# Kernel tuning notes

Hardware: AMD Instinct MI355X
Metric: run time of the kernel (lower is better)

## Reference

```python
import jax, jax.numpy as jnp
import numpy as np

EPS = 1e-3  # matches eps=0.001 in __init__


def p2o(psf, H, W):
    """PSF -> OTF: zero-pad to (H,W), roll so kernel center is at origin, FFT2."""
    B, C, kh, kw = psf.shape
    otf = jnp.zeros((B, C, H, W), psf.dtype).at[:, :, :kh, :kw].set(psf)
    otf = jnp.roll(otf, (-(kh // 2), -(kw // 2)), axis=(-2, -1))
    return jnp.fft.fft2(otf)


def splits_mean(a, sf):
    """Mean over the sf*sf distinct blocks of splits(): contiguous-chunk split
    via view(sf, H/sf, sf, W/sf); mean over the two sf axes equals mean over
    the scale^2 trailing dim of the original splits output."""
    B, C, H, W = a.shape
    return a.reshape(B, C, sf, H // sf, sf, W // sf).mean(axis=(2, 4))


def setup_inputs() -> dict:
    key = jax.random.key(0)
    kx, kk = jax.random.split(key)
    x = jax.random.normal(kx, (4, 64, 128, 128), dtype=jnp.float32)
    k = jax.random.uniform(kk, (4, 64, 25, 25), dtype=jnp.float32)
    alpha = jnp.zeros((1, 64, 1, 1), dtype=jnp.float32)  # learned parameter
    return {"x": x, "k": k, "alpha": alpha, "sf": 2}


def reference(x, k, alpha, sf):
    biaseps = jax.nn.sigmoid(alpha - 9.0) + EPS          # (1,C,1,1)
    B, C, h, w = x.shape
    H, W = h * sf, w * sf
    # s-fold zero-fill upsample (STy)
    STy = jnp.zeros((B, C, H, W), x.dtype).at[:, :, ::sf, ::sf].set(x)
    # nearest-neighbor interpolate by sf
    xu = jnp.repeat(jnp.repeat(x, sf, axis=-2), sf, axis=-1) if sf != 1 else x
    FB = p2o(k, H, W)                                    # complex (B,C,H,W)
    FBC = jnp.conj(FB)
    F2B = jnp.abs(FB) ** 2
    FBFy = FBC * jnp.fft.fft2(STy)
    FR = FBFy + jnp.fft.fft2(biaseps * xu)
    FBR = splits_mean(FB * FR, sf)                       # (B,C,H/sf,W/sf)
    invW = splits_mean(F2B, sf)
    invWBR = FBR / (invW + biaseps)
    FCBinvWBR = FBC * jnp.tile(invWBR, (1, 1, sf, sf))   # repeat(1,1,sf,sf)
    FX = (FR - FCBinvWBR) / biaseps
    return jnp.real(jnp.fft.ifft2(FX))
```

## Files before the change

kernel.cpp:

```cpp
#include <hip/hip_runtime.h>
#include <math.h>


static __device__ __forceinline__ float2 cmul(float2 a, float2 b) {
    return make_float2(a.x * b.x - a.y * b.y, a.x * b.y + a.y * b.x);
}
static __device__ __forceinline__ float2 cadd(float2 a, float2 b) {
    return make_float2(a.x + b.x, a.y + b.y);
}
static __device__ __forceinline__ float2 csub(float2 a, float2 b) {
    return make_float2(a.x - b.x, a.y - b.y);
}
static __device__ __forceinline__ float2 conjf2(float2 a) {
    return make_float2(a.x, -a.y);
}
static __device__ __forceinline__ int PHI(int i) { return i + (i >> 3); }

template <int HB, int SIGN, int THREADS>
static __device__ __forceinline__ void fill_tw(float2* tw) {
    for (int i = threadIdx.x; i < HB; i += THREADS) {
        float s, c;
        __sincosf((float)SIGN * (float)M_PI * (float)i / (float)HB, &s, &c);
        tw[i] = make_float2(c, s);
    }
}

template <int N, int R, int SIGN>
static __device__ __forceinline__ int fft_lds_rows(float2 (&buf)[2][R][N],
                                                   const float2* __restrict__ tw) {
    constexpr int HB = N / 2;
    const int tid = threadIdx.x;
    const int row = tid / HB;
    const int bt = tid % HB;
    int cur = 0, m = 1;
    for (int l = HB; l >= 1; l >>= 1) {
        __syncthreads();
        const int k = bt & (m - 1);
        const float2 w = tw[bt - k];
        float2 a = buf[cur][row][bt];
        float2 b = buf[cur][row][bt + HB];
        float2 d = make_float2(a.x - b.x, a.y - b.y);
        float2 wd = make_float2(w.x * d.x - w.y * d.y, w.x * d.y + w.y * d.x);
        const int o = 2 * bt - k;
        buf[cur ^ 1][row][o] = make_float2(a.x + b.x, a.y + b.y);
        buf[cur ^ 1][row][o + m] = wd;
        cur ^= 1;
        m <<= 1;
    }
    __syncthreads();
    return cur;
}

template <int SIGN, int NCOL>
static __device__ __forceinline__ int fft4_cols_wavelocal(float2 (&buf)[2][NCOL][130],
                                                          const float2* __restrict__ tw) {
    const int lane = threadIdx.x & 63;
    const int wv = threadIdx.x >> 6;
    const int col = wv * 4 + (lane >> 4);
    const int r = lane & 15;
    int cur = 0, m = 1;
#pragma unroll
    for (int st = 0; st < 3; ++st) {
#pragma unroll
        for (int b = 0; b < 2; ++b) {
            const int bq = r + 16 * b;
            const int k = bq & (m - 1);
            const int jm = bq - k;
            const float2 w1 = tw[jm];
            const float2 w2 = tw[2 * jm];
            const float2 w3 = tw[3 * jm];
            float2 a0 = buf[cur][col][bq];
            float2 a1 = buf[cur][col][bq + 32];
            float2 a2 = buf[cur][col][bq + 64];
            float2 a3 = buf[cur][col][bq + 96];
            float2 s02 = cadd(a0, a2), d02 = csub(a0, a2);
            float2 s13 = cadd(a1, a3), d13 = csub(a1, a3);
            float2 b0 = cadd(s02, s13), b2 = csub(s02, s13);
            float2 b1 = make_float2(d02.x - (float)SIGN * d13.y,
                                    d02.y + (float)SIGN * d13.x);
            float2 b3 = make_float2(d02.x + (float)SIGN * d13.y,
                                    d02.y - (float)SIGN * d13.x);
            const int o = 4 * jm + k;
            buf[cur ^ 1][col][o] = b0;
            buf[cur ^ 1][col][o + m] = cmul(w1, b1);
            buf[cur ^ 1][col][o + 2 * m] = cmul(w2, b2);
            buf[cur ^ 1][col][o + 3 * m] = cmul(w3, b3);
        }
        cur ^= 1;
        m <<= 2;
    }
#pragma unroll
    for (int b = 0; b < 4; ++b) {
        const int bt = r + 16 * b;
        float2 a = buf[cur][col][bt];
        float2 bb = buf[cur][col][bt + 64];
        buf[cur ^ 1][col][bt] = cadd(a, bb);
        buf[cur ^ 1][col][bt + 64] = csub(a, bb);
    }
    return cur ^ 1;
}

__global__ __launch_bounds__(256) void k1_fft_rows_x(const float* __restrict__ x,
                                                     float2* __restrict__ Fx) {
    __shared__ float2 buf[2][4][128];
    __shared__ float2 tw64m[64];
    const int tid = threadIdx.x;
    const int row = tid >> 6;
    const int t = tid & 63;
    fill_tw<64, -1, 256>(tw64m);
    const int gpair = blockIdx.x * 4 + row;
    const float* r0 = x + (size_t)gpair * 256;
    const float* r1 = r0 + 128;
    const float2 a0 = ((const float2*)r0)[t];
    const float2 a1 = ((const float2*)r1)[t];
    buf[0][row][2 * t].x = a0.x;
    buf[0][row][2 * t].y = a1.x;
    buf[0][row][2 * t + 1].x = a0.y;
    buf[0][row][2 * t + 1].y = a1.y;
    int cur = fft_lds_rows<128, 4, -1>(buf, tw64m);
    float2* d0 = Fx + (size_t)gpair * 256;
    float2* d1 = d0 + 128;
    for (int h = 0; h < 2; ++h) {
        int tt = t + h * 64;
        if (tt > 64) continue;
        float2 Zt = buf[cur][row][tt];
        float2 Zm = buf[cur][row][(128 - tt) & 127];
        d0[tt] = make_float2(0.5f * (Zt.x + Zm.x), 0.5f * (Zt.y - Zm.y));
        float ax = Zt.x - Zm.x, ay = Zt.y + Zm.y;
        d1[tt] = make_float2(0.5f * ay, -0.5f * ax);
    }
}

__global__ __launch_bounds__(256) void k2_fft_cols_x(float2* __restrict__ Fx) {
    __shared__ float2 buf[2][16][130];
    __shared__ float2 tw[96];
    const int tid = threadIdx.x;
    const int img = blockIdx.x / 5;
    const int c0 = (blockIdx.x % 5) * 16;
    for (int i = tid; i < 96; i += 256) {
        float s, c;
        __sincosf(-(float)M_PI * (float)i / 64.f, &s, &c);
        tw[i] = make_float2(c, s);
    }
    float2* base = Fx + (size_t)img * 16384 + c0;
    for (int it = 0; it < 8; ++it) {
        int idx = it * 256 + tid;
        int rr = idx >> 4, cc = idx & 15;
        buf[0][cc][rr] = base[rr * 128 + cc];
    }
    __syncthreads();
    int cur = fft4_cols_wavelocal<-1, 16>(buf, tw);
    __syncthreads();
    for (int it = 0; it < 8; ++it) {
        int idx = it * 256 + tid;
        int rr = idx >> 4, cc = idx & 15;
        base[rr * 128 + cc] = buf[cur][cc][rr];
    }
}

__global__ __launch_bounds__(128) void k3_fft_rows_k(const float* __restrict__ kin,
                                                     float2* __restrict__ FBtmp) {
    __shared__ float2 buf[2][1][256];
    __shared__ float2 tw128m[128];
    const int tid = threadIdx.x;
    const int img = blockIdx.x / 25;
    const int lr = blockIdx.x % 25;
    fill_tw<128, -1, 128>(tw128m);
    const float* krow = kin + img * 625 + lr * 25;
    for (int h = 0; h < 2; ++h) {
        int v = tid + h * 128;
        int pc = (v + 12) & 255;
        buf[0][0][v] = make_float2(pc < 25 ? krow[pc] : 0.f, 0.f);
    }
    int cur = fft_lds_rows<256, 1, -1>(buf, tw128m);
    float2* dst = FBtmp + (size_t)img * 6400 + lr * 256;
    dst[tid] = buf[cur][0][tid];
    dst[tid + 128] = buf[cur][0][tid + 128];
}

__global__ __launch_bounds__(256, 4) void k6_fused(const float2* __restrict__ FBtmp,
                                                   const float2* __restrict__ Fx,
                                                   const float* __restrict__ alpha,
                                                   float2* __restrict__ Zf) {
    __shared__ float2 sm_buf0[4 * 288];
    __shared__ float2 sm_buf1[4 * 288];
    __shared__ float2 tw[192];
    float2* Tt = sm_buf0;
    float2* stageF = sm_buf1;
    const int tid = threadIdx.x;
    const int rs = tid >> 6;
    const int q = tid & 63;
    const int img = blockIdx.x / 33;
    const int bq = blockIdx.x % 33;
    const int pa = 2 * bq;
    const int pb = (pa + 1 < 65) ? (pa + 1) : 64;

    const float2* src = FBtmp + (size_t)img * 6400 + tid;
    float2 S[25];
#pragma unroll
    for (int p = 0; p < 25; ++p) S[p] = src[p * 256];

    for (int i = tid; i < 192; i += 256) {
        float s, c;
        __sincosf((float)M_PI * (float)i / 128.f, &s, &c);
        tw[i] = make_float2(c, s);
    }
    {
        const float k2pi = -2.f * (float)M_PI / 256.f;
        for (int i = tid; i < 50; i += 256) {
            const int which = i / 25, p = i - which * 25;
            const int u = which ? pb : pa;
            float s, c;
            __sincosf(k2pi * (float)((u * (p + 244)) & 255), &s, &c);
            Tt[which * 25 + p] = make_float2(c, s);
        }
    }
    __syncthreads();

    {
        float2 aA = make_float2(0.f, 0.f), bA = make_float2(0.f, 0.f);
        float2 aB = make_float2(0.f, 0.f), bB = make_float2(0.f, 0.f);
#pragma unroll
        for (int p = 0; p < 25; ++p) {
            const float2 s = S[p];
            const float2 ta = Tt[p];
            const float axx = ta.x * s.x, ayy = ta.y * s.y;
            const float axy = ta.x * s.y, ayx = ta.y * s.x;
            aA.x += axx - ayy;
            aA.y += axy + ayx;
            if (p & 1) {
                bA.x -= axx + ayy;
                bA.y -= axy - ayx;
            } else {
                bA.x += axx + ayy;
                bA.y += axy - ayx;
            }
            const float2 tb = Tt[25 + p];
            const float bxx = tb.x * s.x, byy = tb.y * s.y;
            const float bxy = tb.x * s.y, byx = tb.y * s.x;
            aB.x += bxx - byy;
            aB.y += bxy + byx;
            if (p & 1) {
                bB.x -= bxx + byy;
                bB.y -= bxy - byx;
            } else {
                bB.x += bxx + byy;
                bB.y += bxy - byx;
            }
        }
        stageF[tid] = aA;
        stageF[256 + tid] = bA;
        stageF[512 + tid] = aB;
        stageF[768 + tid] = bB;
    }
    __syncthreads();

    const int p = (rs < 2) ? pa : pb;
    const int sb = rs & 2;
    const int u = ((rs & 1) == 0) ? p : (128 - p);
    const int um = u & 127;
    const int msel = (um == p) ? 0 : 1;
    const int mi = sb | msel;
    const int oi = sb | (1 - msel);

    const float ci = tw[um].x, si = -tw[um].y;
    const float b = 1.f / (1.f + __expf(9.f - alpha[img & 63])) + 1e-3f;
    const float scale = 1.f / 65536.f;
    const float2 Di0 = make_float2(1.f + ci, si);
    const float2 Di1 = make_float2(1.f - ci, -si);
    const float2 Du = (u < 128) ? Di0 : Di1;
#pragma unroll
    for (int h = 0; h < 2; ++h) {
        const int t = q + 64 * h;
        float2 f00 = stageF[mi * 256 + t];
        float2 f01 = stageF[mi * 256 + t + 128];
        float2 f10, f11;
        if (um == 0) {
            f10 = stageF[oi * 256 + t];
            f11 = stageF[oi * 256 + t + 128];
        } else {
            f10 = conjf2(stageF[oi * 256 + ((256 - t) & 255)]);
            f11 = conjf2(stageF[oi * 256 + 128 - t]);
        }
        const bool mir = (t > 64);
        const int rr = mir ? ((128 - um) & 127) : um;
        const int cc = mir ? (128 - t) : t;
        float2 fx = Fx[(size_t)img * 16384 + rr * 128 + cc];
        if (mir) fx.y = -fx.y;
        const float cj = tw[t].x, sj = -tw[t].y;
        float2 Dj0 = make_float2(1.f + cj, sj);
        float2 Dj1 = make_float2(1.f - cj, -sj);
        float2 A = cadd(cmul(f00, Dj0), cmul(f01, Dj1));
        float2 Bt = cadd(cmul(f10, Dj0), cmul(f11, Dj1));
        float2 S1 = cadd(cmul(A, Di0), cmul(Bt, Di1));
        S1.x *= 0.25f;
        S1.y *= 0.25f;
        float S2 = 0.25f * (f00.x * f00.x + f00.y * f00.y + f01.x * f01.x + f01.y * f01.y +
                            f10.x * f10.x + f10.y * f10.y + f11.x * f11.x + f11.y * f11.y);
        float inv = 1.f / (S2 + b);
        float2 mm = make_float2((1.f - S1.x) * inv, (-S1.y) * inv);
        float2 c0v = (u < 128) ? f00 : f10;
        float2 c1v = (u < 128) ? f01 : f11;
        float2 t0 = cadd(cmul(conjf2(c0v), mm), cmul(Du, Dj0));
        float2 t1 = cadd(cmul(conjf2(c1v), mm), cmul(Du, Dj1));
        float2 FX0 = cmul(fx, t0);
        float2 FX1 = cmul(fx, t1);
        sm_buf0[rs * 288 + PHI(t)] = make_float2(FX0.x * scale, FX0.y * scale);
        sm_buf0[rs * 288 + PHI(t + 128)] = make_float2(FX1.x * scale, FX1.y * scale);
    }
    __syncthreads();

    {
        float2* Bc = sm_buf0;
        float2* Bn = sm_buf1;
        int m = 1;
#pragma unroll
        for (int st = 0; st < 3; ++st) {
            const int k = q & (m - 1);
            const int jm = q - k;
            const float2 w1 = tw[jm];
            const float2 w2 = tw[2 * jm];
            const float2 w3 = tw[3 * jm];
            float2 a0 = Bc[rs * 288 + PHI(q)];
            float2 a1 = Bc[rs * 288 + PHI(q + 64)];
            float2 a2 = Bc[rs * 288 + PHI(q + 128)];
            float2 a3 = Bc[rs * 288 + PHI(q + 192)];
            float2 s02 = cadd(a0, a2), d02 = csub(a0, a2);
            float2 s13 = cadd(a1, a3), d13 = csub(a1, a3);
            float2 b0 = cadd(s02, s13), b2v = csub(s02, s13);
            float2 b1 = make_float2(d02.x - d13.y, d02.y + d13.x);
            float2 b3 = make_float2(d02.x + d13.y, d02.y - d13.x);
            const int o = 4 * jm + k;
            Bn[rs * 288 + PHI(o)] = b0;
            Bn[rs * 288 + PHI(o + m)] = cmul(w1, b1);
            Bn[rs * 288 + PHI(o + 2 * m)] = cmul(w2, b2v);
            Bn[rs * 288 + PHI(o + 3 * m)] = cmul(w3, b3);
            float2* tp = Bc; Bc = Bn; Bn = tp;
            m <<= 2;
        }
        {
            float2 a0 = Bc[rs * 288 + PHI(q)];
            float2 a1 = Bc[rs * 288 + PHI(q + 64)];
            float2 a2 = Bc[rs * 288 + PHI(q + 128)];
            float2 a3 = Bc[rs * 288 + PHI(q + 192)];
            float2 s02 = cadd(a0, a2), d02 = csub(a0, a2);
            float2 s13 = cadd(a1, a3), d13 = csub(a1, a3);
            Bc[rs * 288 + PHI(q)] = cadd(s02, s13);
            Bc[rs * 288 + PHI(q + 64)] = make_float2(d02.x - d13.y, d02.y + d13.x);
            Bc[rs * 288 + PHI(q + 128)] = csub(s02, s13);
            Bc[rs * 288 + PHI(q + 192)] = make_float2(d02.x + d13.y, d02.y - d13.x);
        }
    }
    __syncthreads();

    const int u0 = u;
    bool dowrite = ((rs & 1) == 0) ? true : (p > 0 && p < 64);
    if (pb == pa && rs >= 2) dowrite = false;
    if (dowrite) {
        const float2 w = tw[u0];
        float2* zb = Zf + (size_t)img * 32768 + (size_t)u0 * 256;
#pragma unroll
        for (int hh = 0; hh < 4; ++hh) {
            const int jj = q + 64 * hh;
            float2 su = sm_buf1[rs * 288 + PHI(jj)];
            float2 s2 = sm_buf1[(rs ^ 1) * 288 + PHI(jj)];
            float2 e = make_float2(su.x + s2.x, su.y - s2.y);
            float2 o_ = make_float2(su.x - s2.x, su.y + s2.y);
            float2 wo = cmul(w, o_);
            zb[jj] = make_float2(e.x - wo.y, e.y + wo.x);
        }
    }
}

__global__ __launch_bounds__(256) void k7_c2r(const float2* __restrict__ Zf,
                                              float* __restrict__ out) {
    __shared__ float2 buf[2][16][130];
    __shared__ float2 tw[96];
    const int tid = threadIdx.x;
    const int img = blockIdx.x >> 4;
    const int c0 = (blockIdx.x & 15) * 16;
    for (int i = tid; i < 96; i += 256) {
        float s, c;
        __sincosf((float)M_PI * (float)i / 64.f, &s, &c);
        tw[i] = make_float2(c, s);
    }
    const float2* zb = Zf + (size_t)img * 32768 + c0;
    for (int it = 0; it < 8; ++it) {
        int idx = it * 256 + tid;
        int rr = idx >> 4, cc = idx & 15;
        buf[0][cc][rr] = zb[rr * 256 + cc];
    }
    __syncthreads();
    int cur = fft4_cols_wavelocal<1, 16>(buf, tw);
    __syncthreads();
    float* ob = out + (size_t)img * 65536 + c0;
    for (int it = 0; it < 8; ++it) {
        int idx = it * 256 + tid;
        int n = idx >> 4, c = idx & 15;
        float2 y = buf[cur][c][n];
        ob[(2 * n) * 256 + c] = y.x;
        ob[(2 * n + 1) * 256 + c] = y.y;
    }
}

extern "C" void kernel_launch(void* const* d_in, const int* in_sizes, int n_in,
                              void* d_out, int out_size, void* d_ws, size_t ws_size,
                              hipStream_t stream) {
    const float* x = (const float*)d_in[0];
    const float* k = (const float*)d_in[1];
    const float* alpha = (const float*)d_in[2];
    float* out = (float*)d_out;

    float2* Fx = (float2*)d_ws;
    float2* Zf = Fx + 256 * 16384;
    float2* FBtmp = Zf + 256 * 32768;

    hipLaunchKernelGGL(k1_fft_rows_x, dim3(4096), dim3(256), 0, stream, x, Fx);
    hipLaunchKernelGGL(k2_fft_cols_x, dim3(256 * 5), dim3(256), 0, stream, Fx);
    hipLaunchKernelGGL(k3_fft_rows_k, dim3(6400), dim3(128), 0, stream, k, FBtmp);
    hipLaunchKernelGGL(k6_fused, dim3(256 * 33), dim3(256), 0, stream, FBtmp, Fx, alpha, Zf);
    hipLaunchKernelGGL(k7_c2r, dim3(4096), dim3(256), 0, stream, Zf, out);
}
```

Before: 181.3 us.

## Merge x-row and kernel-row FFT launches, register-fuse first FFT stage in k6

Fuses the row FFTs of x and of the PSF into one launch by splitting on block index, with two PSF rows per 256-thread block. This removes one kernel launch and the 128-thread small-block inefficiency. Inside k6_fused, the first radix-4 stage of the 256-point FFT now runs in registers straight from the computed spectrum values, with vectorised float4 LDS writes. It also drops the syncthreads between the later radix-4 stages, uses a new padding function, and reuses each thread's own results in registers during the final write. The wave-local stages without barriers rely on each row being handled by exactly one wavefront, and the k-path blocks do some dead work on padded rows.

```diff
diff --git a/kernel.cpp b/kernel.cpp
--- a/kernel.cpp
+++ b/kernel.cpp
@@ -14,7 +14,7 @@
 static __device__ __forceinline__ float2 conjf2(float2 a) {
     return make_float2(a.x, -a.y);
 }
-static __device__ __forceinline__ int PHI(int i) { return i + (i >> 3); }
+static __device__ __forceinline__ int PHI16(int i) { return i + ((i >> 4) << 1); }
 
 template <int HB, int SIGN, int THREADS>
 static __device__ __forceinline__ void fill_tw(float2* tw) {
@@ -100,34 +100,65 @@
     return cur ^ 1;
 }
 
-__global__ __launch_bounds__(256) void k1_fft_rows_x(const float* __restrict__ x,
-                                                     float2* __restrict__ Fx) {
-    __shared__ float2 buf[2][4][128];
-    __shared__ float2 tw64m[64];
+__global__ __launch_bounds__(256) void k13(const float* __restrict__ x,
+                                           const float* __restrict__ kin,
+                                           float2* __restrict__ Fx,
+                                           float2* __restrict__ FBtmp) {
+    __shared__ __align__(16) float2 pool[1152];
     const int tid = threadIdx.x;
-    const int row = tid >> 6;
-    const int t = tid & 63;
-    fill_tw<64, -1, 256>(tw64m);
-    const int gpair = blockIdx.x * 4 + row;
-    const float* r0 = x + (size_t)gpair * 256;
-    const float* r1 = r0 + 128;
-    const float2 a0 = ((const float2*)r0)[t];
-    const float2 a1 = ((const float2*)r1)[t];
-    buf[0][row][2 * t].x = a0.x;
-    buf[0][row][2 * t].y = a1.x;
-    buf[0][row][2 * t + 1].x = a0.y;
-    buf[0][row][2 * t + 1].y = a1.y;
-    int cur = fft_lds_rows<128, 4, -1>(buf, tw64m);
-    float2* d0 = Fx + (size_t)gpair * 256;
-    float2* d1 = d0 + 128;
-    for (int h = 0; h < 2; ++h) {
-        int tt = t + h * 64;
-        if (tt > 64) continue;
-        float2 Zt = buf[cur][row][tt];
-        float2 Zm = buf[cur][row][(128 - tt) & 127];
-        d0[tt] = make_float2(0.5f * (Zt.x + Zm.x), 0.5f * (Zt.y - Zm.y));
-        float ax = Zt.x - Zm.x, ay = Zt.y + Zm.y;
-        d1[tt] = make_float2(0.5f * ay, -0.5f * ax);
+    if (blockIdx.x < 4096) {
+        using Buf1 = float2[2][4][128];
+        Buf1& buf = *reinterpret_cast<Buf1*>(pool);
+        float2* tw64m = pool + 1024;
+        const int row = tid >> 6;
+        const int t = tid & 63;
+        fill_tw<64, -1, 256>(tw64m);
+        const int gpair = blockIdx.x * 4 + row;
+        const float* r0 = x + (size_t)gpair * 256;
+        const float* r1 = r0 + 128;
+        const float2 a0 = ((const float2*)r0)[t];
+        const float2 a1 = ((const float2*)r1)[t];
+        buf[0][row][2 * t].x = a0.x;
+        buf[0][row][2 * t].y = a1.x;
+        buf[0][row][2 * t + 1].x = a0.y;
+        buf[0][row][2 * t + 1].y = a1.y;
+        int cur = fft_lds_rows<128, 4, -1>(buf, tw64m);
+        float2* d0 = Fx + (size_t)gpair * 256;
+        float2* d1 = d0 + 128;
+        for (int h = 0; h < 2; ++h) {
+            int tt = t + h * 64;
+            if (tt > 64) continue;
+            float2 Zt = buf[cur][row][tt];
+            float2 Zm = buf[cur][row][(128 - tt) & 127];
+            d0[tt] = make_float2(0.5f * (Zt.x + Zm.x), 0.5f * (Zt.y - Zm.y));
+            float ax = Zt.x - Zm.x, ay = Zt.y + Zm.y;
+            d1[tt] = make_float2(0.5f * ay, -0.5f * ax);
+        }
+    } else {
+        using Buf3 = float2[2][2][256];
+        Buf3& buf = *reinterpret_cast<Buf3*>(pool);
+        float2* tw128m = pool + 1024;
+        const int b3 = blockIdx.x - 4096;
+        const int img = b3 / 13;
+        const int sub = b3 % 13;
+        const int row = tid >> 7;
+        const int t2 = tid & 127;
+        int lr = sub * 2 + row;
+        const bool live = (lr < 25);
+        if (!live) lr = 24;
+        fill_tw<128, -1, 256>(tw128m);
+        const float* krow = kin + img * 625 + lr * 25;
+        for (int h = 0; h < 2; ++h) {
+            int v = t2 + h * 128;
+            int pc = (v + 12) & 255;
+            buf[0][row][v] = make_float2(pc < 25 ? krow[pc] : 0.f, 0.f);
+        }
+        int cur = fft_lds_rows<256, 2, -1>(buf, tw128m);
+        if (live) {
+            float2* dst = FBtmp + (size_t)img * 6400 + lr * 256;
+            dst[t2] = buf[cur][row][t2];
+            dst[t2 + 128] = buf[cur][row][t2 + 128];
+        }
     }
 }
 
@@ -158,32 +189,12 @@
     }
 }
 
-__global__ __launch_bounds__(128) void k3_fft_rows_k(const float* __restrict__ kin,
-                                                     float2* __restrict__ FBtmp) {
-    __shared__ float2 buf[2][1][256];
-    __shared__ float2 tw128m[128];
-    const int tid = threadIdx.x;
-    const int img = blockIdx.x / 25;
-    const int lr = blockIdx.x % 25;
-    fill_tw<128, -1, 128>(tw128m);
-    const float* krow = kin + img * 625 + lr * 25;
-    for (int h = 0; h < 2; ++h) {
-        int v = tid + h * 128;
-        int pc = (v + 12) & 255;
-        buf[0][0][v] = make_float2(pc < 25 ? krow[pc] : 0.f, 0.f);
-    }
-    int cur = fft_lds_rows<256, 1, -1>(buf, tw128m);
-    float2* dst = FBtmp + (size_t)img * 6400 + lr * 256;
-    dst[tid] = buf[cur][0][tid];
-    dst[tid + 128] = buf[cur][0][tid + 128];
-}
-
 __global__ __launch_bounds__(256, 4) void k6_fused(const float2* __restrict__ FBtmp,
                                                    const float2* __restrict__ Fx,
                                                    const float* __restrict__ alpha,
                                                    float2* __restrict__ Zf) {
-    __shared__ float2 sm_buf0[4 * 288];
-    __shared__ float2 sm_buf1[4 * 288];
+    __shared__ __align__(16) float2 sm_buf0[4 * 288];
+    __shared__ __align__(16) float2 sm_buf1[4 * 288];
     __shared__ float2 tw[192];
     float2* Tt = sm_buf0;
     float2* stageF = sm_buf1;
@@ -269,6 +280,7 @@
     const float2 Di0 = make_float2(1.f + ci, si);
     const float2 Di1 = make_float2(1.f - ci, -si);
     const float2 Du = (u < 128) ? Di0 : Di1;
+    float2 X0, X1, X2, X3;
 #pragma unroll
     for (int h = 0; h < 2; ++h) {
         const int t = q + 64 * h;
@@ -305,52 +317,77 @@
         float2 t1 = cadd(cmul(conjf2(c1v), mm), cmul(Du, Dj1));
         float2 FX0 = cmul(fx, t0);
         float2 FX1 = cmul(fx, t1);
-        sm_buf0[rs * 288 + PHI(t)] = make_float2(FX0.x * scale, FX0.y * scale);
-        sm_buf0[rs * 288 + PHI(t + 128)] = make_float2(FX1.x * scale, FX1.y * scale);
-    }
-    __syncthreads();
-
-    {
-        float2* Bc = sm_buf0;
-        float2* Bn = sm_buf1;
-        int m = 1;
-#pragma unroll
-        for (int st = 0; st < 3; ++st) {
-            const int k = q & (m - 1);
-            const int jm = q - k;
-            const float2 w1 = tw[jm];
-            const float2 w2 = tw[2 * jm];
-            const float2 w3 = tw[3 * jm];
-            float2 a0 = Bc[rs * 288 + PHI(q)];
-            float2 a1 = Bc[rs * 288 + PHI(q + 64)];
-            float2 a2 = Bc[rs * 288 + PHI(q + 128)];
-            float2 a3 = Bc[rs * 288 + PHI(q + 192)];
-            float2 s02 = cadd(a0, a2), d02 = csub(a0, a2);
-            float2 s13 = cadd(a1, a3), d13 = csub(a1, a3);
-            float2 b0 = cadd(s02, s13), b2v = csub(s02, s13);
-            float2 b1 = make_float2(d02.x - d13.y, d02.y + d13.x);
-            float2 b3 = make_float2(d02.x + d13.y, d02.y - d13.x);
-            const int o = 4 * jm + k;
-            Bn[rs * 288 + PHI(o)] = b0;
-            Bn[rs * 288 + PHI(o + m)] = cmul(w1, b1);
-            Bn[rs * 288 + PHI(o + 2 * m)] = cmul(w2, b2v);
-            Bn[rs * 288 + PHI(o + 3 * m)] = cmul(w3, b3);
-            float2* tp = Bc; Bc = Bn; Bn = tp;
-            m <<= 2;
-        }
-        {
-            float2 a0 = Bc[rs * 288 + PHI(q)];
-            float2 a1 = Bc[rs * 288 + PHI(q + 64)];
-            float2 a2 = Bc[rs * 288 + PHI(q + 128)];
-            float2 a3 = Bc[rs * 288 + PHI(q + 192)];
-            float2 s02 = cadd(a0, a2), d02 = csub(a0, a2);
-            float2 s13 = cadd(a1, a3), d13 = csub(a1, a3);
-            Bc[rs * 288 + PHI(q)] = cadd(s02, s13);
-            Bc[rs * 288 + PHI(q + 64)] = make_float2(d02.x - d13.y, d02.y + d13.x);
-            Bc[rs * 288 + PHI(q + 128)] = csub(s02, s13);
-            Bc[rs * 288 + PHI(q + 192)] = make_float2(d02.x + d13.y, d02.y - d13.x);
-        }
-    }
+        FX0.x *= scale; FX0.y *= scale;
+        FX1.x *= scale; FX1.y *= scale;
+        if (h == 0) { X0 = FX0; X2 = FX1; } else { X1 = FX0; X3 = FX1; }
+    }
+
+    {
+        float2 s02 = cadd(X0, X2), d02 = csub(X0, X2);
+        float2 s13 = cadd(X1, X3), d13 = csub(X1, X3);
+        float2 b0 = cadd(s02, s13), b2v = csub(s02, s13);
+        float2 b1 = make_float2(d02.x - d13.y, d02.y + d13.x);
+        float2 b3 = make_float2(d02.x + d13.y, d02.y - d13.x);
+        float2 c1 = cmul(tw[q], b1);
+        float2 c2 = cmul(tw[2 * q], b2v);
+        float2 c3 = cmul(tw[3 * q], b3);
+        float4* dst4 = reinterpret_cast<float4*>(&sm_buf0[rs * 288 + PHI16(4 * q)]);
+        dst4[0] = make_float4(b0.x, b0.y, c1.x, c1.y);
+        dst4[1] = make_float4(c2.x, c2.y, c3.x, c3.y);
+    }
+    __syncthreads();
+
+    {
+        const int k4 = q & 3, jm = q - k4;
+        float2 a0 = sm_buf0[rs * 288 + PHI16(q)];
+        float2 a1 = sm_buf0[rs * 288 + PHI16(q + 64)];
+        float2 a2 = sm_buf0[rs * 288 + PHI16(q + 128)];
+        float2 a3 = sm_buf0[rs * 288 + PHI16(q + 192)];
+        float2 s02 = cadd(a0, a2), d02 = csub(a0, a2);
+        float2 s13 = cadd(a1, a3), d13 = csub(a1, a3);
+        float2 b0 = cadd(s02, s13), b2v = csub(s02, s13);
+        float2 b1 = make_float2(d02.x - d13.y, d02.y + d13.x);
+        float2 b3 = make_float2(d02.x + d13.y, d02.y - d13.x);
+        const int o = 4 * jm + k4;
+        sm_buf1[rs * 288 + PHI16(o)] = b0;
+        sm_buf1[rs * 288 + PHI16(o + 4)] = cmul(tw[jm], b1);
+        sm_buf1[rs * 288 + PHI16(o + 8)] = cmul(tw[2 * jm], b2v);
+        sm_buf1[rs * 288 + PHI16(o + 12)] = cmul(tw[3 * jm], b3);
+    }
+    {
+        const int k16 = q & 15, jm = q - k16;
+        float2 a0 = sm_buf1[rs * 288 + PHI16(q)];
+        float2 a1 = sm_buf1[rs * 288 + PHI16(q + 64)];
+        float2 a2 = sm_buf1[rs * 288 + PHI16(q + 128)];
+        float2 a3 = sm_buf1[rs * 288 + PHI16(q + 192)];
+        float2 s02 = cadd(a0, a2), d02 = csub(a0, a2);
+        float2 s13 = cadd(a1, a3), d13 = csub(a1, a3);
+        float2 b0 = cadd(s02, s13), b2v = csub(s02, s13);
+        float2 b1 = make_float2(d02.x - d13.y, d02.y + d13.x);
+        float2 b3 = make_float2(d02.x + d13.y, d02.y - d13.x);
+        const int o = 4 * jm + k16;
+        sm_buf0[rs * 288 + PHI16(o)] = b0;
+        sm_buf0[rs * 288 + PHI16(o + 16)] = cmul(tw[jm], b1);
+        sm_buf0[rs * 288 + PHI16(o + 32)] = cmul(tw[2 * jm], b2v);
+        sm_buf0[rs * 288 + PHI16(o + 48)] = cmul(tw[3 * jm], b3);
+    }
+    float2 Y0, Y1, Y2, Y3;
+    {
+        float2 a0 = sm_buf0[rs * 288 + PHI16(q)];
+        float2 a1 = sm_buf0[rs * 288 + PHI16(q + 64)];
+        float2 a2 = sm_buf0[rs * 288 + PHI16(q + 128)];
+        float2 a3 = sm_buf0[rs * 288 + PHI16(q + 192)];
+        float2 s02 = cadd(a0, a2), d02 = csub(a0, a2);
+        float2 s13 = cadd(a1, a3), d13 = csub(a1, a3);
+        Y0 = cadd(s02, s13);
+        Y1 = make_float2(d02.x - d13.y, d02.y + d13.x);
+        Y2 = csub(s02, s13);
+        Y3 = make_float2(d02.x + d13.y, d02.y - d13.x);
+    }
+    sm_buf1[rs * 288 + PHI16(q)] = Y0;
+    sm_buf1[rs * 288 + PHI16(q + 64)] = Y1;
+    sm_buf1[rs * 288 + PHI16(q + 128)] = Y2;
+    sm_buf1[rs * 288 + PHI16(q + 192)] = Y3;
     __syncthreads();
 
     const int u0 = u;
@@ -359,11 +396,12 @@
     if (dowrite) {
         const float2 w = tw[u0];
         float2* zb = Zf + (size_t)img * 32768 + (size_t)u0 * 256;
+        float2 own[4] = {Y0, Y1, Y2, Y3};
 #pragma unroll
         for (int hh = 0; hh < 4; ++hh) {
             const int jj = q + 64 * hh;
-            float2 su = sm_buf1[rs * 288 + PHI(jj)];
-            float2 s2 = sm_buf1[(rs ^ 1) * 288 + PHI(jj)];
+            float2 su = own[hh];
+            float2 s2 = sm_buf1[(rs ^ 1) * 288 + PHI16(jj)];
             float2 e = make_float2(su.x + s2.x, su.y - s2.y);
             float2 o_ = make_float2(su.x - s2.x, su.y + s2.y);
             float2 wo = cmul(w, o_);
@@ -415,9 +453,8 @@
     float2* Zf = Fx + 256 * 16384;
     float2* FBtmp = Zf + 256 * 32768;
 
-    hipLaunchKernelGGL(k1_fft_rows_x, dim3(4096), dim3(256), 0, stream, x, Fx);
+    hipLaunchKernelGGL(k13, dim3(4096 + 256 * 13), dim3(256), 0, stream, x, k, Fx, FBtmp);
     hipLaunchKernelGGL(k2_fft_cols_x, dim3(256 * 5), dim3(256), 0, stream, Fx);
-    hipLaunchKernelGGL(k3_fft_rows_k, dim3(6400), dim3(128), 0, stream, k, FBtmp);
     hipLaunchKernelGGL(k6_fused, dim3(256 * 33), dim3(256), 0, stream, FBtmp, Fx, alpha, Zf);
     hipLaunchKernelGGL(k7_c2r, dim3(4096), dim3(256), 0, stream, Zf, out);
 }
```

After: 178.8 us. Within noise of the previous version (-1.4%).
